# Kernel tuning notes

Measured on AMD Instinct MI355X. Metric: run time of the kernel, lower is better.

Reference implementation:

```python
import jax, jax.numpy as jnp
import numpy as np

K = 16
EPS = 1e-5

def _conv1x1(w, b, x):
    # w: [O, I], x: [B, I, N] -> [B, O, N]
    return jnp.einsum('oi,bin->bon', w, x) + b[None, :, None]

def _bn(g, be, m, v, x):
    # inference-mode batchnorm over channel dim of [B, C, N]
    inv = g / jnp.sqrt(v + EPS)
    return x * inv[None, :, None] + (be - m * inv)[None, :, None]

def setup_inputs() -> dict:
    key = jax.random.key(0)
    ks = jax.random.split(key, 16)
    B, C, N = 2, 128, 8192
    d = {}
    d['x'] = jax.random.normal(ks[0], (B, C, N), jnp.float32)
    d['xyz'] = jax.random.normal(ks[1], (B, N, 3), jnp.float32)
    def conv(k, o, i):
        k1, k2 = jax.random.split(k)
        s = 1.0 / np.sqrt(i)
        return (jax.random.uniform(k1, (o, i), jnp.float32, -s, s),
                jax.random.uniform(k2, (o,), jnp.float32, -s, s))
    def bn(k, c):
        return (jax.random.uniform(k, (c,), jnp.float32, 0.5, 1.5),
                jnp.zeros((c,), jnp.float32), jnp.zeros((c,), jnp.float32), jnp.ones((c,), jnp.float32))
    # boundary_net: 2C->C (bn,relu), C->C (bn,relu)
    d['bw1'], d['bb1'] = conv(ks[2], C, 2 * C)
    d['bn1g'], d['bn1b'], d['bn1m'], d['bn1v'] = bn(ks[3], C)
    d['bw2'], d['bb2'] = conv(ks[4], C, C)
    d['bn2g'], d['bn2b'], d['bn2m'], d['bn2v'] = bn(ks[5], C)
    # spatial_relation: 4->32 (bn,relu), 32->64
    d['sw1'], d['sb1'] = conv(ks[6], 32, 4)
    d['sbng'], d['sbnb'], d['sbnm'], d['sbnv'] = bn(ks[7], 32)
    d['sw2'], d['sb2'] = conv(ks[8], 64, 32)
    # attention: C+64 -> C//2 (bn,relu), C//2 -> C, sigmoid
    d['aw1'], d['ab1'] = conv(ks[9], C // 2, C + 64)
    d['abng'], d['abnb'], d['abnm'], d['abnv'] = bn(ks[10], C // 2)
    d['aw2'], d['ab2'] = conv(ks[11], C, C // 2)
    return d

def reference(x, xyz, bw1, bb1, bn1g, bn1b, bn1m, bn1v, bw2, bb2, bn2g, bn2b, bn2m, bn2v,
              sw1, sb1, sbng, sbnb, sbnm, sbnv, sw2, sb2,
              aw1, ab1, abng, abnb, abnm, abnv, aw2, ab2):
    B, C, N = x.shape
    # pairwise squared distances [B, N, N]
    xx = jnp.sum(xyz * xyz, axis=2)  # [B, N]
    dist = xx[:, :, None] + xx[:, None, :] - 2.0 * jnp.einsum('bnd,bmd->bnm', xyz, xyz)
    _, knn_idx = jax.lax.top_k(-dist, K)  # [B, N, K], K smallest distances
    # gather neighbor coords [B, N, K, 3]
    knn_xyz = jax.vmap(lambda p, i: p[i])(xyz, knn_idx)
    rel = knn_xyz - xyz[:, :, None, :]                  # [B, N, K, 3]
    rel_d = jnp.sqrt(jnp.sum(rel * rel, axis=-1))       # [B, N, K]
    mean_rel = jnp.mean(rel, axis=2).transpose(0, 2, 1)   # [B, 3, N]
    mean_d = jnp.mean(rel_d, axis=2)[:, None, :]           # [B, 1, N]
    spatial = jnp.concatenate([mean_rel, mean_d], axis=1)  # [B, 4, N]
    s = jax.nn.relu(_bn(sbng, sbnb, sbnm, sbnv, _conv1x1(sw1, sb1, spatial)))
    spatial_feat = _conv1x1(sw2, sb2, s)  # [B, 64, N]
    # gather neighbor features [B, C, N, K]
    knn_feat = jax.vmap(lambda xb, ib: xb[:, ib])(x, knn_idx)
    max_diff = jnp.max(knn_feat - x[:, :, :, None], axis=3)  # [B, C, N]
    bf = jnp.concatenate([x, max_diff], axis=1)  # [B, 2C, N]
    bf = jax.nn.relu(_bn(bn1g, bn1b, bn1m, bn1v, _conv1x1(bw1, bb1, bf)))
    boundary_feat = jax.nn.relu(_bn(bn2g, bn2b, bn2m, bn2v, _conv1x1(bw2, bb2, bf)))
    ai = jnp.concatenate([x, spatial_feat], axis=1)  # [B, C+64, N]
    a = jax.nn.relu(_bn(abng, abnb, abnm, abnv, _conv1x1(aw1, ab1, ai)))
    attn = jax.nn.sigmoid(_conv1x1(aw2, ab2, a))  # [B, C, N]
    return x + boundary_feat * attn
```

## Files before the change

kernel.cpp:

```cpp
#include <hip/hip_runtime.h>
#include <math.h>

#define NPTS  8192
#define NB    2
#define NTOT  (NPTS*NB)
#define GD    60
#define NCELL (GD*GD*GD)
#define TOTC  (NB*NCELL)
#define HCELL 0.2f
#define INVH  5.0f
#define ORGN  (-6.0f)
#define NN    8192
#define SCAN_CHUNK 1024
#define NBLK_SCAN  ((TOTC + SCAN_CHUNK - 1) / SCAN_CHUNK)
#define RSTART    2
#define RESC      4
#define SEL_CAP  1024

#define OFF_CNT     ((size_t)0)
#define OFF_OFFS    (OFF_CNT    + (size_t)TOTC*4)
#define OFF_CELLID  (OFF_OFFS   + (size_t)TOTC*4)
#define OFF_RANK    (OFF_CELLID + (size_t)NTOT*4)
#define OFF_SPOS    (OFF_RANK   + (size_t)NTOT*4)
#define OFF_KNN     (OFF_SPOS   + (size_t)NTOT*16)
#define OFF_SPATIAL (OFF_KNN    + (size_t)NTOT*16*4)
#define OFF_XT      (OFF_SPATIAL+ (size_t)NB*4*NPTS*4)
#define OFF_MD      (OFF_XT     + (size_t)NB*128*NPTS*4)
#define OFF_S1      (OFF_MD     + (size_t)NB*128*NPTS*4)
#define OFF_SF      (OFF_S1     + (size_t)NB*32*NPTS*4)
#define OFF_Y1      (OFF_SF     + (size_t)NB*64*NPTS*4)
#define OFF_Y2      (OFF_Y1     + (size_t)NB*128*NPTS*4)
#define OFF_A1      (OFF_Y2     + (size_t)NB*128*NPTS*4)
#define OFF_SC      (OFF_A1     + (size_t)NB*64*NPTS*4)
#define OFF_BSUM    (OFF_SC     + (size_t)1088*4)
#define OFF_BPRE    (OFF_BSUM   + (size_t)NBLK_SCAN*4)
#define OFF_RNG     (((OFF_BPRE + (size_t)NBLK_SCAN*4) + 15) & ~(size_t)15)

static __device__ __forceinline__ float sumsq3(float x, float y, float z) {
    return __fadd_rn(__fadd_rn(__fmul_rn(x, x), __fmul_rn(y, y)), __fmul_rn(z, z));
}
static __device__ __forceinline__ float pdist4(float qx, float qy, float qz, float qxx,
                                               float px, float py, float pz) {
    float pxx = sumsq3(px, py, pz);
    float dot = __fadd_rn(__fadd_rn(__fmul_rn(qx, px), __fmul_rn(qy, py)), __fmul_rn(qz, pz));
    return __fsub_rn(__fadd_rn(qxx, pxx), __fadd_rn(dot, dot));
}
static __device__ __forceinline__ unsigned fkey(float f) {
    unsigned b = __float_as_uint(f);
    return b ^ ((unsigned)(((int)b) >> 31) | 0x80000000u);
}
static __device__ __forceinline__ unsigned long long shflx64(unsigned long long v, int m) {
    unsigned lo = __shfl_xor((unsigned)v, m, 64);
    unsigned hi = __shfl_xor((unsigned)(v >> 32), m, 64);
    return ((unsigned long long)hi << 32) | lo;
}
static __device__ __forceinline__ int wave_scan_incl(int v, int lane) {
    #pragma unroll
    for (int d = 1; d < 64; d <<= 1) {
        int u = __shfl_up(v, d, 64);
        v += (lane >= d) ? u : 0;
    }
    return v;
}
static __device__ __forceinline__ unsigned long long tkmake(float m) {
    return ((unsigned long long)(fkey(__fsub_rn(__fmul_rn(m, m), 1e-4f)) + 1u)) << 27;
}

__global__ void cell_build(const float* __restrict__ xyz, int* __restrict__ cnt,
                           int* __restrict__ cellid, int* __restrict__ rank) {
    int t = blockIdx.x * 256 + threadIdx.x;
    if (t >= NTOT) return;
    const float* p = xyz + (size_t)t * 3;
    float x = p[0], y = p[1], z = p[2];
    int cx = min(GD - 1, max(0, (int)floorf((x - ORGN) * INVH)));
    int cy = min(GD - 1, max(0, (int)floorf((y - ORGN) * INVH)));
    int cz = min(GD - 1, max(0, (int)floorf((z - ORGN) * INVH)));
    int gcell = (t >> 13) * NCELL + (cz * GD + cy) * GD + cx;
    rank[t] = atomicAdd(&cnt[gcell], 1);
    cellid[t] = gcell;
}

__global__ __launch_bounds__(256) void scan_sums(const int* __restrict__ cnt, int* __restrict__ bsum) {
    __shared__ int red[256];
    int blk = blockIdx.x, t = threadIdx.x;
    int i0 = blk * SCAN_CHUNK + t * 4;
    int s = 0;
    if (i0 + 3 < TOTC) {
        int4 v = *(const int4*)(cnt + i0);
        s = v.x + v.y + v.z + v.w;
    } else {
        for (int j = 0; j < 4; ++j) if (i0 + j < TOTC) s += cnt[i0 + j];
    }
    red[t] = s;
    __syncthreads();
    for (int d = 128; d > 0; d >>= 1) {
        if (t < d) red[t] += red[t + d];
        __syncthreads();
    }
    if (t == 0) bsum[blk] = red[0];
}

__global__ __launch_bounds__(512) void scan_top(const int* __restrict__ bsum, int* __restrict__ bpre) {
    __shared__ int ps[512];
    int t = threadIdx.x;
    int v = (t < NBLK_SCAN) ? bsum[t] : 0;
    ps[t] = v;
    __syncthreads();
    for (int d = 1; d < 512; d <<= 1) {
        int u = 0;
        if (t >= d) u = ps[t - d];
        __syncthreads();
        ps[t] += u;
        __syncthreads();
    }
    if (t < NBLK_SCAN) bpre[t] = ps[t] - v;
}

__global__ __launch_bounds__(256) void scan_write(const int* __restrict__ cnt, const int* __restrict__ bpre,
                                                  int* __restrict__ offs, int2* __restrict__ rng) {
    __shared__ int ps[256];
    int blk = blockIdx.x, t = threadIdx.x;
    int i0 = blk * SCAN_CHUNK + t * 4;
    int a = 0, b = 0, c = 0, d = 0;
    if (i0 + 3 < TOTC) {
        int4 v = *(const int4*)(cnt + i0);
        a = v.x; b = v.y; c = v.z; d = v.w;
    } else {
        if (i0 + 0 < TOTC) a = cnt[i0 + 0];
        if (i0 + 1 < TOTC) b = cnt[i0 + 1];
        if (i0 + 2 < TOTC) c = cnt[i0 + 2];
        if (i0 + 3 < TOTC) d = cnt[i0 + 3];
    }
    int s = a + b + c + d;
    ps[t] = s;
    __syncthreads();
    for (int dd = 1; dd < 256; dd <<= 1) {
        int u = 0;
        if (t >= dd) u = ps[t - dd];
        __syncthreads();
        ps[t] += u;
        __syncthreads();
    }
    int base = bpre[blk] + ps[t] - s;
    if (i0 + 3 < TOTC) {
        offs[i0 + 0] = base;
        offs[i0 + 1] = base + a;
        offs[i0 + 2] = base + a + b;
        offs[i0 + 3] = base + a + b + c;
        *(int4*)(rng + i0)     = make_int4(base, base + a, base + a, base + a + b);
        *(int4*)(rng + i0 + 2) = make_int4(base + a + b, base + a + b + c,
                                           base + a + b + c, base + s);
    } else {
        if (i0 + 0 < TOTC) { offs[i0 + 0] = base;             rng[i0 + 0] = make_int2(base, base + a); }
        if (i0 + 1 < TOTC) { offs[i0 + 1] = base + a;         rng[i0 + 1] = make_int2(base + a, base + a + b); }
        if (i0 + 2 < TOTC) { offs[i0 + 2] = base + a + b;     rng[i0 + 2] = make_int2(base + a + b, base + a + b + c); }
        if (i0 + 3 < TOTC) { offs[i0 + 3] = base + a + b + c; rng[i0 + 3] = make_int2(base + a + b + c, base + s); }
    }
}

__global__ void scatter_k(const float* __restrict__ xyz, const int* __restrict__ cellid,
                          const int* __restrict__ rank, const int* __restrict__ offs,
                          float4* __restrict__ spos) {
    int t = blockIdx.x * 256 + threadIdx.x;
    if (t >= NTOT) return;
    const float* p = xyz + (size_t)t * 3;
    float x = p[0], y = p[1], z = p[2];
    int pos = offs[cellid[t]] + rank[t];
    spos[pos] = make_float4(x, y, z, __int_as_float(t & (NPTS - 1)));
}

__global__ __launch_bounds__(64) void knn_kernel(const float4* __restrict__ spos,
                                                 const int2* __restrict__ rng,
                                                 int* __restrict__ knn,
                                                 float* __restrict__ spatial) {
    __shared__ __align__(16) unsigned long long sel[SEL_CAP];
    __shared__ __align__(16) unsigned long long sel2[512];
    int lane = threadIdx.x;
    int bid  = blockIdx.x;
    int s = (int)(__brev((unsigned)bid) >> 18);
    float4 q = spos[s];
    float qx = q.x, qy = q.y, qz = q.z;
    float qxx = sumsq3(qx, qy, qz);
    int b  = s >> 13;
    int nq = __float_as_int(q.w);
    int cx = min(GD - 1, max(0, (int)floorf((qx - ORGN) * INVH)));
    int cy = min(GD - 1, max(0, (int)floorf((qy - ORGN) * INVH)));
    int cz = min(GD - 1, max(0, (int)floorf((qz - ORGN) * INVH)));
    const int2* rg = rng + b * NCELL;

    float mlx = qx - (ORGN + (float)cx * HCELL);
    float mhx = (ORGN + (float)(cx + 1) * HCELL) - qx;
    float mly = qy - (ORGN + (float)cy * HCELL);
    float mhy = (ORGN + (float)(cy + 1) * HCELL) - qy;
    float mlz = qz - (ORGN + (float)cz * HCELL);
    float mhz = (ORGN + (float)(cz + 1) * HCELL) - qz;
    float margin0 = fminf(fminf(fminf(mlx, mhx), fminf(mly, mhy)), fminf(mlz, mhz));

    int tot = 0, ovf = 0;

    auto scan_ball = [&](int RB, float mfin, unsigned long long tkfin) {
        if (mfin <= 0.f) return;
        float mfin2 = mfin * mfin;
        int L = 2 * RB + 1, nrows = L * L;
        for (int r0 = 0; r0 < nrows; r0 += 64) {
            int nr = min(64, nrows - r0);
            int rr = r0 + lane;
            int num = 0, start = 0;
            if (rr < nrows) {
                int dzr = rr / L - RB, dyr = rr % L - RB;
                int zc = cz + dzr, yc = cy + dyr;
                if ((unsigned)zc < GD && (unsigned)yc < GD) {
                    float ylo = ORGN + (float)yc * HCELL;
                    float zlo = ORGN + (float)zc * HCELL;
                    float dyl = fmaxf(fmaxf(ylo - qy, qy - (ylo + HCELL)), 0.f);
                    float dzl = fmaxf(fmaxf(zlo - qz, qz - (zlo + HCELL)), 0.f);
                    float rem = mfin2 - dyl * dyl - dzl * dzl;
                    if (rem > -1e-4f) {
                        float xh = sqrtf(fmaxf(rem, 0.f)) + 1e-3f;
                        int xlo = max(0, (int)floorf((qx - xh - ORGN) * INVH));
                        int xhi = min(GD - 1, (int)floorf((qx + xh - ORGN) * INVH));
                        if (xlo <= xhi) {
                            int rowb = (zc * GD + yc) * GD;
                            start = rg[rowb + xlo].x;
                            num   = rg[rowb + xhi].y - start;
                        }
                    }
                }
            }
            int inc = wave_scan_incl(num, lane);
            int ctot = __shfl(inc, 63, 64);
            if (ctot == 0) continue;
            int excl = inc - num;
            auto eg = [&](int base, int& sv, float4& pv, bool& vld) {
                int t = base + lane;
                vld = t < ctot;
                int tc = vld ? t : (ctot - 1);
                int lo = 0, hi = nr - 1;
                #pragma unroll
                for (int st = 0; st < 6; ++st) {
                    int mid = (lo + hi + 1) >> 1;
                    int e = __shfl(excl, mid, 64);
                    bool g = (e <= tc);
                    lo = g ? mid : lo;
                    hi = g ? hi : (mid - 1);
                }
                sv = __shfl(start, lo, 64) + (tc - __shfl(excl, lo, 64));
                pv = spos[sv];
            };
            int s0; float4 p0; bool v0;
            eg(0, s0, p0, v0);
            for (int base = 0; base < ctot; base += 64) {
                int s1 = 0; float4 p1 = p0; bool v1 = false;
                if (base + 64 < ctot) eg(base + 64, s1, p1, v1);
                float d = pdist4(qx, qy, qz, qxx, p0.x, p0.y, p0.z);
                unsigned long long key = ((unsigned long long)fkey(d) << 27)
                                       | ((unsigned long long)(unsigned)__float_as_int(p0.w) << 14)
                                       | (unsigned)s0;
                bool pass = v0 && (key < tkfin);
                unsigned long long mk = __ballot(pass);
                int cnum = (int)__popcll(mk);
                if (tot + cnum > SEL_CAP) { ovf = 1; return; }
                if (pass) sel[tot + (int)__popcll(mk & ((1ULL << lane) - 1ULL))] = key;
                tot += cnum;
                s0 = s1; p0 = p1; v0 = v1;
            }
        }
    };

    auto count_below = [&](unsigned long long tk) {
        int c = 0;
        for (int t0 = 0; t0 < tot; t0 += 64) {
            int tt = t0 + lane;
            if (tt < tot) c += (sel[tt] < tk) ? 1 : 0;
        }
        for (int o = 32; o > 0; o >>= 1) c += __shfl_xor(c, o, 64);
        return c;
    };

    float mfin1 = margin0 + (float)RSTART * HCELL;
    unsigned long long tkf1 = (mfin1 > 0.f) ? tkmake(mfin1) : 0ULL;
    if (tkf1) scan_ball(RSTART, mfin1, tkf1);

    unsigned long long tkey_sel = ~0ULL;
    int csel = 0;
    bool have = false;
    if (!ovf && tot >= 16) {
        float mA = margin0 + 1.0f * HCELL;
        if (mA > 0.f) {
            unsigned long long tkA = tkmake(mA);
            int cA = count_below(tkA);
            if (cA >= 16) { tkey_sel = tkA; csel = cA; have = true; }
        }
        if (!have) { tkey_sel = ~0ULL; csel = tot; have = true; }
    }
    if (!have && !ovf) {
        tot = 0;
        float mfin4 = margin0 + (float)RESC * HCELL;
        unsigned long long tkf4 = (mfin4 > 0.f) ? tkmake(mfin4) : 0ULL;
        if (tkf4) scan_ball(RESC, mfin4, tkf4);
        if (!ovf && tot >= 16) {
            float mB = margin0 + (float)(RESC - 1) * HCELL;
            if (mB > 0.f) {
                unsigned long long tkB = tkmake(mB);
                int cB = count_below(tkB);
                if (cB >= 16) { tkey_sel = tkB; csel = cB; have = true; }
            }
            if (!have) { tkey_sel = ~0ULL; csel = tot; have = true; }
        }
    }

    if (!have) {
        const float LADR[16] = {0.35f, 0.4725f, 0.637875f, 0.86113125f,
                                1.1625272f, 1.5694117f, 2.1187058f, 2.8602529f,
                                3.8613414f, 5.2128109f, 7.0372947f, 9.5003478f,
                                12.825470f, 17.314384f, 23.374418f, 31.555464f};
        int sbase = b << 13;
        int cc[16];
        #pragma unroll
        for (int k = 0; k < 16; ++k) cc[k] = 0;
        for (int i0 = 0; i0 < NPTS; i0 += 64) {
            float4 p = spos[sbase + i0 + lane];
            float d = pdist4(qx, qy, qz, qxx, p.x, p.y, p.z);
            #pragma unroll
            for (int k = 0; k < 16; ++k) cc[k] += (d < LADR[k] * LADR[k]) ? 1 : 0;
        }
        #pragma unroll
        for (int k = 0; k < 16; ++k)
            for (int o = 32; o > 0; o >>= 1) cc[k] += __shfl_xor(cc[k], o, 64);
        float Tq = LADR[15] * LADR[15]; int cL = cc[15];
        #pragma unroll
        for (int k = 14; k >= 0; --k) if (cc[k] >= 16) { Tq = LADR[k] * LADR[k]; cL = cc[k]; }
        if (cL <= SEL_CAP) {
            tot = 0;
            for (int i0 = 0; i0 < NPTS; i0 += 64) {
                int idx = sbase + i0 + lane;
                float4 p = spos[idx];
                float d = pdist4(qx, qy, qz, qxx, p.x, p.y, p.z);
                bool pass = (d < Tq);
                unsigned long long key = ((unsigned long long)fkey(d) << 27)
                                       | ((unsigned long long)(unsigned)__float_as_int(p.w) << 14)
                                       | (unsigned)idx;
                unsigned long long mk = __ballot(pass);
                if (pass) sel[tot + (int)__popcll(mk & ((1ULL << lane) - 1ULL))] = key;
                tot += (int)__popcll(mk);
            }
            tkey_sel = ~0ULL;
            csel = tot;
        } else {
            unsigned long long* mybuf = sel + lane;
            unsigned long long minkey = ~0ULL, maxkey = 0;
            int nbuf = 0;
            for (int i = lane; i < NPTS; i += 64) {
                float4 p = spos[sbase + i];
                float d = pdist4(qx, qy, qz, qxx, p.x, p.y, p.z);
                unsigned long long key = ((unsigned long long)fkey(d) << 27)
                                       | ((unsigned long long)(unsigned)__float_as_int(p.w) << 14)
                                       | (unsigned)(sbase + i);
                if (nbuf < 16) {
                    mybuf[(size_t)nbuf * 64] = key;
                    ++nbuf;
                    minkey = (key < minkey) ? key : minkey;
                    maxkey = (key > maxkey) ? key : maxkey;
                } else if (key < maxkey) {
                    unsigned long long vmax = 0, v2 = 0;
                    int pmax = 0;
                    #pragma unroll
                    for (int j = 0; j < 16; ++j) {
                        unsigned long long v = mybuf[(size_t)j * 64];
                        if (v > vmax) { v2 = vmax; vmax = v; pmax = j; }
                        else if (v > v2) { v2 = v; }
                    }
                    mybuf[(size_t)pmax * 64] = key;
                    maxkey = (key > v2) ? key : v2;
                    minkey = (key < minkey) ? key : minkey;
                }
            }
            unsigned long long keep = ~0ULL;
            for (int k = 0; k < 16; ++k) {
                unsigned long long m = minkey;
                for (int o = 32; o > 0; o >>= 1) {
                    unsigned long long pv = shflx64(m, o);
                    m = (pv < m) ? pv : m;
                }
                unsigned long long bal = __ballot(minkey == m);
                int wl = __ffsll((long long)bal) - 1;
                if (lane == wl) {
                    int pos = 0;
                    for (int j = 0; j < nbuf; ++j) if (mybuf[(size_t)j * 64] == m) pos = j;
                    --nbuf;
                    mybuf[(size_t)pos * 64] = mybuf[(size_t)nbuf * 64];
                    unsigned long long nm = ~0ULL;
                    for (int j = 0; j < nbuf; ++j) {
                        unsigned long long v = mybuf[(size_t)j * 64];
                        nm = (v < nm) ? v : nm;
                    }
                    minkey = nm;
                }
                if (lane == k) keep = m;
            }
            float rx = 0.f, ry = 0.f, rz = 0.f, rd = 0.f;
            if (lane < 16) {
                int sp = (int)(keep & 0x3FFFu);
                int oi = (int)((keep >> 14) & 0x1FFFu);
                float4 p = spos[sp];
                rx = p.x - qx; ry = p.y - qy; rz = p.z - qz;
                rd = sqrtf(__fadd_rn(__fadd_rn(__fmul_rn(rx, rx), __fmul_rn(ry, ry)), __fmul_rn(rz, rz)));
                knn[(((size_t)b << 13) + nq) * 16 + lane] = oi;
            }
            for (int o = 8; o > 0; o >>= 1) {
                rx += __shfl_xor(rx, o, 64);
                ry += __shfl_xor(ry, o, 64);
                rz += __shfl_xor(rz, o, 64);
                rd += __shfl_xor(rd, o, 64);
            }
            if (lane == 0) {
                const float inv16 = 0.0625f;
                spatial[((size_t)b * 4 + 0) * NPTS + nq] = rx * inv16;
                spatial[((size_t)b * 4 + 1) * NPTS + nq] = ry * inv16;
                spatial[((size_t)b * 4 + 2) * NPTS + nq] = rz * inv16;
                spatial[((size_t)b * 4 + 3) * NPTS + nq] = rd * inv16;
            }
            return;
        }
    }

    const unsigned long long* src = sel;
    int m = tot;
    if (tkey_sel != ~0ULL && csel <= 512) {
        int w = 0;
        for (int t0 = 0; t0 < tot; t0 += 64) {
            int tt = t0 + lane;
            unsigned long long v = (tt < tot) ? sel[tt] : ~0ULL;
            bool pass = (tt < tot) && (v < tkey_sel);
            unsigned long long mk = __ballot(pass);
            if (pass) sel2[w + (int)__popcll(mk & ((1ULL << lane) - 1ULL))] = v;
            w += (int)__popcll(mk);
        }
        asm volatile("s_waitcnt lgkmcnt(0)" ::: "memory");
        __builtin_amdgcn_sched_barrier(0);
        src = sel2; m = w;
        tkey_sel = ~0ULL;
    }
    float rxs = 0.f, rys = 0.f, rzs = 0.f, rds = 0.f;
    for (int t0 = 0; t0 < m; t0 += 64) {
        int tt = t0 + lane;
        if (tt < m) {
            unsigned long long kt = src[tt];
            if (kt < tkey_sel) {
                int rr = 0;
                for (int j = 0; j < m; ++j) rr += (src[j] < kt) ? 1 : 0;
                if (rr < 16) {
                    int sp = (int)(kt & 0x3FFFu);
                    int oi = (int)((kt >> 14) & 0x1FFFu);
                    float4 p = spos[sp];
                    float dx = p.x - qx, dy = p.y - qy, dz = p.z - qz;
                    float dl = sqrtf(__fadd_rn(__fadd_rn(__fmul_rn(dx, dx), __fmul_rn(dy, dy)), __fmul_rn(dz, dz)));
                    knn[(((size_t)b << 13) + nq) * 16 + rr] = oi;
                    rxs += dx; rys += dy; rzs += dz; rds += dl;
                }
            }
        }
    }
    for (int o = 32; o > 0; o >>= 1) {
        rxs += __shfl_xor(rxs, o, 64);
        rys += __shfl_xor(rys, o, 64);
        rzs += __shfl_xor(rzs, o, 64);
        rds += __shfl_xor(rds, o, 64);
    }
    if (lane == 0) {
        const float inv16 = 0.0625f;
        spatial[((size_t)b * 4 + 0) * NPTS + nq] = rxs * inv16;
        spatial[((size_t)b * 4 + 1) * NPTS + nq] = rys * inv16;
        spatial[((size_t)b * 4 + 2) * NPTS + nq] = rzs * inv16;
        spatial[((size_t)b * 4 + 3) * NPTS + nq] = rds * inv16;
    }
}

__global__ void transpose_k(const float* __restrict__ x, float* __restrict__ xT) {
    __shared__ float tl[32][33];
    int b = blockIdx.z;
    int n0 = blockIdx.x * 32, c0 = blockIdx.y * 32;
    int tx = threadIdx.x, ty = threadIdx.y;
    const float* xb = x + (size_t)b * 128 * NN;
    float* xtb = xT + (size_t)b * NN * 128;
    for (int i = 0; i < 32; i += 8) tl[ty + i][tx] = xb[(size_t)(c0 + ty + i) * NN + n0 + tx];
    __syncthreads();
    for (int i = 0; i < 32; i += 8) xtb[(size_t)(n0 + ty + i) * 128 + c0 + tx] = tl[tx][ty + i];
}

__global__ __launch_bounds__(256) void md_k(const float* __restrict__ xT,
                                            const int* __restrict__ knn,
                                            float* __restrict__ md) {
    __shared__ int ki[8][16];
    __shared__ float smd[8][132];
    int b = blockIdx.y;
    int n0 = blockIdx.x * 8;
    int tid = threadIdx.x;
    if (tid < 128) ki[tid >> 4][tid & 15] = knn[(((size_t)b << 13) + n0 + (tid >> 4)) * 16 + (tid & 15)];
    __syncthreads();
    int nl = tid >> 5;
    int c4 = (tid & 31) * 4;
    const float* xb = xT + (size_t)b * NPTS * 128;
    float4 m = make_float4(-3.0e38f, -3.0e38f, -3.0e38f, -3.0e38f);
    #pragma unroll
    for (int k = 0; k < 16; ++k) {
        const float4 g = *(const float4*)(xb + (size_t)ki[nl][k] * 128 + c4);
        m.x = fmaxf(m.x, g.x); m.y = fmaxf(m.y, g.y); m.z = fmaxf(m.z, g.z); m.w = fmaxf(m.w, g.w);
    }
    const float4 own = *(const float4*)(xb + (size_t)(n0 + nl) * 128 + c4);
    m.x -= own.x; m.y -= own.y; m.z -= own.z; m.w -= own.w;
    *(float4*)(&smd[nl][c4]) = m;
    __syncthreads();
    for (int r = 0; r < 4; ++r) {
        int c = (tid >> 3) + 32 * r;
        int n2 = tid & 7;
        md[((size_t)b * 128 + c) * NN + n0 + n2] = smd[n2][c];
    }
}

__global__ void prep_k(const float* bb1, const float* g1, const float* be1, const float* m1, const float* v1,
                       const float* bb2, const float* g2, const float* be2, const float* m2, const float* v2,
                       const float* sb1, const float* gs,  const float* bes, const float* ms, const float* vs,
                       const float* sb2,
                       const float* ab1, const float* ga,  const float* bea, const float* ma, const float* va,
                       const float* ab2, float* sc) {
    int t = threadIdx.x;
    if (t < 128) {
        float i1 = g1[t] / sqrtf(v1[t] + 1e-5f);
        sc[t] = i1;        sc[128 + t] = bb1[t] * i1 + be1[t] - m1[t] * i1;
        float i2 = g2[t] / sqrtf(v2[t] + 1e-5f);
        sc[256 + t] = i2;  sc[384 + t] = bb2[t] * i2 + be2[t] - m2[t] * i2;
        sc[832 + t] = 1.0f; sc[960 + t] = ab2[t];
    }
    if (t < 32) {
        float is = gs[t] / sqrtf(vs[t] + 1e-5f);
        sc[512 + t] = is;  sc[544 + t] = sb1[t] * is + bes[t] - ms[t] * is;
    }
    if (t < 64) {
        sc[576 + t] = 1.0f; sc[640 + t] = sb2[t];
        float ia = ga[t] / sqrtf(va[t] + 1e-5f);
        sc[704 + t] = ia;  sc[768 + t] = ab1[t] * ia + bea[t] - ma[t] * ia;
    }
}

template <int O, int K, int TILE_N, int SPLIT, int ACT>
__global__ __launch_bounds__(256) void conv_bn(const float* __restrict__ srcA,
                                               const float* __restrict__ srcB,
                                               const float* __restrict__ W,
                                               const float* __restrict__ scale,
                                               const float* __restrict__ shift,
                                               float* __restrict__ out) {
    constexpr int KC  = (K < 64) ? K : 64;
    constexpr int NT4 = TILE_N / 4;
    constexpr int O4  = O / 4;
    static_assert(NT4 * O4 == 256, "thread mapping");
    __shared__ float wT[KC][O + 4];
    __shared__ float inT[KC][TILE_N];
    int tid = threadIdx.x;
    int b = blockIdx.z;
    int n0 = blockIdx.x * TILE_N;
    int n_thr = tid % NT4;
    int o_thr = tid / NT4;
    float acc[4][4] = {{0.f, 0.f, 0.f, 0.f}, {0.f, 0.f, 0.f, 0.f}, {0.f, 0.f, 0.f, 0.f}, {0.f, 0.f, 0.f, 0.f}};

    for (int k0 = 0; k0 < K; k0 += KC) {
        for (int idx = tid; idx < KC * O; idx += 256) {
            int cc = idx % KC;
            int o  = idx / KC;
            wT[cc][o] = W[(size_t)o * K + k0 + cc];
        }
        for (int idx = tid; idx < KC * NT4; idx += 256) {
            int cc = idx / NT4;
            int nf = idx % NT4;
            int cg = k0 + cc;
            const float* src = (cg < SPLIT)
                ? (srcA + ((size_t)b * SPLIT + cg) * NN)
                : (srcB + ((size_t)b * (K - SPLIT) + (cg - SPLIT)) * NN);
            *(float4*)(&inT[cc][nf * 4]) = *(const float4*)(src + n0 + nf * 4);
        }
        __syncthreads();
        #pragma unroll 8
        for (int c = 0; c < KC; ++c) {
            float4 wv = *(const float4*)(&wT[c][o_thr * 4]);
            float4 iv = *(const float4*)(&inT[c][n_thr * 4]);
            acc[0][0] = fmaf(wv.x, iv.x, acc[0][0]); acc[0][1] = fmaf(wv.x, iv.y, acc[0][1]);
            acc[0][2] = fmaf(wv.x, iv.z, acc[0][2]); acc[0][3] = fmaf(wv.x, iv.w, acc[0][3]);
            acc[1][0] = fmaf(wv.y, iv.x, acc[1][0]); acc[1][1] = fmaf(wv.y, iv.y, acc[1][1]);
            acc[1][2] = fmaf(wv.y, iv.z, acc[1][2]); acc[1][3] = fmaf(wv.y, iv.w, acc[1][3]);
            acc[2][0] = fmaf(wv.z, iv.x, acc[2][0]); acc[2][1] = fmaf(wv.z, iv.y, acc[2][1]);
            acc[2][2] = fmaf(wv.z, iv.z, acc[2][2]); acc[2][3] = fmaf(wv.z, iv.w, acc[2][3]);
            acc[3][0] = fmaf(wv.w, iv.x, acc[3][0]); acc[3][1] = fmaf(wv.w, iv.y, acc[3][1]);
            acc[3][2] = fmaf(wv.w, iv.z, acc[3][2]); acc[3][3] = fmaf(wv.w, iv.w, acc[3][3]);
        }
        __syncthreads();
    }
    #pragma unroll
    for (int j = 0; j < 4; ++j) {
        int o = o_thr * 4 + j;
        float scv = scale[o], shv = shift[o];
        float4 v;
        v.x = fmaf(acc[j][0], scv, shv);
        v.y = fmaf(acc[j][1], scv, shv);
        v.z = fmaf(acc[j][2], scv, shv);
        v.w = fmaf(acc[j][3], scv, shv);
        size_t obase = ((size_t)b * O + o) * NN + n0 + n_thr * 4;
        if (ACT == 1) {
            v.x = fmaxf(v.x, 0.f); v.y = fmaxf(v.y, 0.f); v.z = fmaxf(v.z, 0.f); v.w = fmaxf(v.w, 0.f);
        }
        *(float4*)(out + obase) = v;
    }
}

#define FMA16(ACCV, WV, IV) \
    ACCV[0][0] = fmaf(WV.x, IV.x, ACCV[0][0]); ACCV[0][1] = fmaf(WV.x, IV.y, ACCV[0][1]); \
    ACCV[0][2] = fmaf(WV.x, IV.z, ACCV[0][2]); ACCV[0][3] = fmaf(WV.x, IV.w, ACCV[0][3]); \
    ACCV[1][0] = fmaf(WV.y, IV.x, ACCV[1][0]); ACCV[1][1] = fmaf(WV.y, IV.y, ACCV[1][1]); \
    ACCV[1][2] = fmaf(WV.y, IV.z, ACCV[1][2]); ACCV[1][3] = fmaf(WV.y, IV.w, ACCV[1][3]); \
    ACCV[2][0] = fmaf(WV.z, IV.x, ACCV[2][0]); ACCV[2][1] = fmaf(WV.z, IV.y, ACCV[2][1]); \
    ACCV[2][2] = fmaf(WV.z, IV.z, ACCV[2][2]); ACCV[2][3] = fmaf(WV.z, IV.w, ACCV[2][3]); \
    ACCV[3][0] = fmaf(WV.w, IV.x, ACCV[3][0]); ACCV[3][1] = fmaf(WV.w, IV.y, ACCV[3][1]); \
    ACCV[3][2] = fmaf(WV.w, IV.z, ACCV[3][2]); ACCV[3][3] = fmaf(WV.w, IV.w, ACCV[3][3])

__global__ __launch_bounds__(256) void fused_boundary(const float* __restrict__ x,
                                                      const float* __restrict__ md,
                                                      const float* __restrict__ W1,
                                                      const float* __restrict__ W2,
                                                      const float* __restrict__ sc,
                                                      float* __restrict__ y2b) {
    __shared__ float wT[64][132];
    __shared__ float inT[64][32];
    __shared__ float y1t[128][32];
    int tid = threadIdx.x;
    int b = blockIdx.z;
    int n0 = blockIdx.x * 32;
    int n_thr = tid % 8;
    int o_thr = tid / 8;
    float acc[4][4] = {{0.f,0.f,0.f,0.f},{0.f,0.f,0.f,0.f},{0.f,0.f,0.f,0.f},{0.f,0.f,0.f,0.f}};

    for (int k0 = 0; k0 < 256; k0 += 64) {
        for (int idx = tid; idx < 64 * 128; idx += 256) {
            int cc = idx % 64;
            int o  = idx / 64;
            wT[cc][o] = W1[(size_t)o * 256 + k0 + cc];
        }
        for (int idx = tid; idx < 64 * 8; idx += 256) {
            int cc = idx / 8;
            int nf = idx % 8;
            int cg = k0 + cc;
            const float* src = (cg < 128)
                ? (x  + ((size_t)b * 128 + cg) * NN)
                : (md + ((size_t)b * 128 + (cg - 128)) * NN);
            *(float4*)(&inT[cc][nf * 4]) = *(const float4*)(src + n0 + nf * 4);
        }
        __syncthreads();
        #pragma unroll 8
        for (int c = 0; c < 64; ++c) {
            float4 wv = *(const float4*)(&wT[c][o_thr * 4]);
            float4 iv = *(const float4*)(&inT[c][n_thr * 4]);
            FMA16(acc, wv, iv);
        }
        __syncthreads();
    }
    #pragma unroll
    for (int j = 0; j < 4; ++j) {
        int o = o_thr * 4 + j;
        float scv = sc[o], shv = sc[128 + o];
        float4 v;
        v.x = fmaxf(fmaf(acc[j][0], scv, shv), 0.f);
        v.y = fmaxf(fmaf(acc[j][1], scv, shv), 0.f);
        v.z = fmaxf(fmaf(acc[j][2], scv, shv), 0.f);
        v.w = fmaxf(fmaf(acc[j][3], scv, shv), 0.f);
        *(float4*)(&y1t[o][n_thr * 4]) = v;
    }
    __syncthreads();

    float a2[4][4] = {{0.f,0.f,0.f,0.f},{0.f,0.f,0.f,0.f},{0.f,0.f,0.f,0.f},{0.f,0.f,0.f,0.f}};
    for (int k0 = 0; k0 < 128; k0 += 64) {
        for (int idx = tid; idx < 64 * 128; idx += 256) {
            int cc = idx % 64;
            int o  = idx / 64;
            wT[cc][o] = W2[(size_t)o * 128 + k0 + cc];
        }
        __syncthreads();
        #pragma unroll 8
        for (int c = 0; c < 64; ++c) {
            float4 wv = *(const float4*)(&wT[c][o_thr * 4]);
            float4 iv = *(const float4*)(&y1t[k0 + c][n_thr * 4]);
            FMA16(a2, wv, iv);
        }
        __syncthreads();
    }
    #pragma unroll
    for (int j = 0; j < 4; ++j) {
        int o = o_thr * 4 + j;
        float scv = sc[256 + o], shv = sc[384 + o];
        float4 v;
        v.x = fmaxf(fmaf(a2[j][0], scv, shv), 0.f);
        v.y = fmaxf(fmaf(a2[j][1], scv, shv), 0.f);
        v.z = fmaxf(fmaf(a2[j][2], scv, shv), 0.f);
        v.w = fmaxf(fmaf(a2[j][3], scv, shv), 0.f);
        *(float4*)(y2b + ((size_t)b * 128 + o) * NN + n0 + n_thr * 4) = v;
    }
}

__global__ __launch_bounds__(256) void fused_attn(const float* __restrict__ x,
                                                  const float* __restrict__ sfb,
                                                  const float* __restrict__ W1,
                                                  const float* __restrict__ W2,
                                                  const float* __restrict__ sc,
                                                  const float* __restrict__ y2b,
                                                  float* __restrict__ dout) {
    __shared__ float wT[64][68];
    __shared__ float inT[64][64];
    __shared__ float a1t[64][64];
    int tid = threadIdx.x;
    int b = blockIdx.z;
    int n0 = blockIdx.x * 64;
    int n_thr = tid % 16;
    int o_thr = tid / 16;
    float acc[4][4] = {{0.f,0.f,0.f,0.f},{0.f,0.f,0.f,0.f},{0.f,0.f,0.f,0.f},{0.f,0.f,0.f,0.f}};

    for (int k0 = 0; k0 < 192; k0 += 64) {
        for (int idx = tid; idx < 64 * 64; idx += 256) {
            int cc = idx % 64;
            int o  = idx / 64;
            wT[cc][o] = W1[(size_t)o * 192 + k0 + cc];
        }
        for (int idx = tid; idx < 64 * 16; idx += 256) {
            int cc = idx / 16;
            int nf = idx % 16;
            int cg = k0 + cc;
            const float* src = (cg < 128)
                ? (x   + ((size_t)b * 128 + cg) * NN)
                : (sfb + ((size_t)b * 64 + (cg - 128)) * NN);
            *(float4*)(&inT[cc][nf * 4]) = *(const float4*)(src + n0 + nf * 4);
        }
        __syncthreads();
        #pragma unroll 8
        for (int c = 0; c < 64; ++c) {
            float4 wv = *(const float4*)(&wT[c][o_thr * 4]);
            float4 iv = *(const float4*)(&inT[c][n_thr * 4]);
            FMA16(acc, wv, iv);
        }
        __syncthreads();
    }
    #pragma unroll
    for (int j = 0; j < 4; ++j) {
        int o = o_thr * 4 + j;
        float scv = sc[704 + o], shv = sc[768 + o];
        float4 v;
        v.x = fmaxf(fmaf(acc[j][0], scv, shv), 0.f);
        v.y = fmaxf(fmaf(acc[j][1], scv, shv), 0.f);
        v.z = fmaxf(fmaf(acc[j][2], scv, shv), 0.f);
        v.w = fmaxf(fmaf(acc[j][3], scv, shv), 0.f);
        *(float4*)(&a1t[o][n_thr * 4]) = v;
    }
    __syncthreads();

    for (int oh = 0; oh < 128; oh += 64) {
        for (int idx = tid; idx < 64 * 64; idx += 256) {
            int cc = idx % 64;
            int o  = idx / 64;
            wT[cc][o] = W2[(size_t)(oh + o) * 64 + cc];
        }
        __syncthreads();
        float a2[4][4] = {{0.f,0.f,0.f,0.f},{0.f,0.f,0.f,0.f},{0.f,0.f,0.f,0.f},{0.f,0.f,0.f,0.f}};
        #pragma unroll 8
        for (int c = 0; c < 64; ++c) {
            float4 wv = *(const float4*)(&wT[c][o_thr * 4]);
            float4 iv = *(const float4*)(&a1t[c][n_thr * 4]);
            FMA16(a2, wv, iv);
        }
        #pragma unroll
        for (int j = 0; j < 4; ++j) {
            int o = oh + o_thr * 4 + j;
            float scv = sc[832 + o], shv = sc[960 + o];
            float4 v;
            v.x = fmaf(a2[j][0], scv, shv);
            v.y = fmaf(a2[j][1], scv, shv);
            v.z = fmaf(a2[j][2], scv, shv);
            v.w = fmaf(a2[j][3], scv, shv);
            size_t obase = ((size_t)b * 128 + o) * NN + n0 + n_thr * 4;
            float4 xr = *(const float4*)(x + obase);
            float4 yr = *(const float4*)(y2b + obase);
            v.x = xr.x + yr.x / (1.f + __expf(-v.x));
            v.y = xr.y + yr.y / (1.f + __expf(-v.y));
            v.z = xr.z + yr.z / (1.f + __expf(-v.z));
            v.w = xr.w + yr.w / (1.f + __expf(-v.w));
            *(float4*)(dout + obase) = v;
        }
        __syncthreads();
    }
}

extern "C" void kernel_launch(void* const* d_in, const int* in_sizes, int n_in,
                              void* d_out, int out_size, void* d_ws, size_t ws_size,
                              hipStream_t stream) {
    (void)in_sizes; (void)n_in; (void)out_size; (void)ws_size;
    const float* x    = (const float*)d_in[0];
    const float* xyz  = (const float*)d_in[1];
    const float* bw1  = (const float*)d_in[2];
    const float* bb1  = (const float*)d_in[3];
    const float* bn1g = (const float*)d_in[4];
    const float* bn1b = (const float*)d_in[5];
    const float* bn1m = (const float*)d_in[6];
    const float* bn1v = (const float*)d_in[7];
    const float* bw2  = (const float*)d_in[8];
    const float* bb2  = (const float*)d_in[9];
    const float* bn2g = (const float*)d_in[10];
    const float* bn2b = (const float*)d_in[11];
    const float* bn2m = (const float*)d_in[12];
    const float* bn2v = (const float*)d_in[13];
    const float* sw1  = (const float*)d_in[14];
    const float* sb1  = (const float*)d_in[15];
    const float* sbng = (const float*)d_in[16];
    const float* sbnb = (const float*)d_in[17];
    const float* sbnm = (const float*)d_in[18];
    const float* sbnv = (const float*)d_in[19];
    const float* sw2  = (const float*)d_in[20];
    const float* sb2  = (const float*)d_in[21];
    const float* aw1  = (const float*)d_in[22];
    const float* ab1  = (const float*)d_in[23];
    const float* abng = (const float*)d_in[24];
    const float* abnb = (const float*)d_in[25];
    const float* abnm = (const float*)d_in[26];
    const float* abnv = (const float*)d_in[27];
    const float* aw2  = (const float*)d_in[28];
    const float* ab2  = (const float*)d_in[29];

    char* ws = (char*)d_ws;
    int*    cnt    = (int*)(ws + OFF_CNT);
    int*    offs   = (int*)(ws + OFF_OFFS);
    int*    cellid = (int*)(ws + OFF_CELLID);
    int*    rank   = (int*)(ws + OFF_RANK);
    float4* spos   = (float4*)(ws + OFF_SPOS);
    int*    knn    = (int*)(ws + OFF_KNN);
    float*  spat   = (float*)(ws + OFF_SPATIAL);
    float*  xT     = (float*)(ws + OFF_XT);
    float*  md     = (float*)(ws + OFF_MD);
    float*  s1b    = (float*)(ws + OFF_S1);
    float*  sfb    = (float*)(ws + OFF_SF);
    float*  y2b    = (float*)(ws + OFF_Y2);
    float*  sc     = (float*)(ws + OFF_SC);
    int*    bsum   = (int*)(ws + OFF_BSUM);
    int*    bpre   = (int*)(ws + OFF_BPRE);
    int2*   rng    = (int2*)(ws + OFF_RNG);
    float*  dout   = (float*)d_out;

    hipMemsetAsync(cnt, 0, (size_t)TOTC * 4, stream);
    cell_build<<<dim3((NTOT + 255) / 256), 256, 0, stream>>>(xyz, cnt, cellid, rank);
    scan_sums<<<dim3(NBLK_SCAN), 256, 0, stream>>>(cnt, bsum);
    scan_top<<<dim3(1), 512, 0, stream>>>(bsum, bpre);
    scan_write<<<dim3(NBLK_SCAN), 256, 0, stream>>>(cnt, bpre, offs, rng);
    scatter_k<<<dim3((NTOT + 255) / 256), 256, 0, stream>>>(xyz, cellid, rank, offs, spos);
    knn_kernel<<<dim3(NTOT), 64, 0, stream>>>(spos, rng, knn, spat);
    transpose_k<<<dim3(NPTS / 32, 128 / 32, NB), dim3(32, 8), 0, stream>>>(x, xT);
    md_k<<<dim3(NPTS / 8, NB), 256, 0, stream>>>(xT, knn, md);
    prep_k<<<1, 128, 0, stream>>>(bb1, bn1g, bn1b, bn1m, bn1v,
                                  bb2, bn2g, bn2b, bn2m, bn2v,
                                  sb1, sbng, sbnb, sbnm, sbnv,
                                  sb2,
                                  ab1, abng, abnb, abnm, abnv,
                                  ab2, sc);
    conv_bn<32, 4, 128, 4, 1><<<dim3(NPTS / 128, 1, NB), 256, 0, stream>>>(
        spat, spat, sw1, sc + 512, sc + 544, s1b);
    conv_bn<64, 32, 64, 32, 0><<<dim3(NPTS / 64, 1, NB), 256, 0, stream>>>(
        s1b, s1b, sw2, sc + 576, sc + 640, sfb);
    fused_boundary<<<dim3(NPTS / 32, 1, NB), 256, 0, stream>>>(x, md, bw1, bw2, sc, y2b);
    fused_attn<<<dim3(NPTS / 64, 1, NB), 256, 0, stream>>>(x, sfb, aw1, aw2, sc, y2b, dout);
}
```

Before: 321.4 us.

## Process two kNN queries per wavefront using half-wave sub-groups

The kNN kernel now assigns one query to each 32-lane half of a 64-lane wave, so each block handles two queries and the launch uses half as many blocks. All scans, ballots, shuffles and reductions are narrowed to width 32. The shared selection buffers are split per half, which halves their capacity, and the query-to-block mapping changes from bit-reversed to a strided interleave. The goal is to stop wasting lanes when a query's candidate rows and points do not fill 64 lanes. The risks are that the two halves diverge and get serialized, and that the smaller buffers send more queries to the slow fallback path.

```diff
diff --git a/kernel.cpp b/kernel.cpp
--- a/kernel.cpp
+++ b/kernel.cpp
@@ -15,7 +15,7 @@
 #define NBLK_SCAN  ((TOTC + SCAN_CHUNK - 1) / SCAN_CHUNK)
 #define RSTART    2
 #define RESC      4
-#define SEL_CAP  1024
+#define SEL_CAP_H 512
 
 #define OFF_CNT     ((size_t)0)
 #define OFF_OFFS    (OFF_CNT    + (size_t)TOTC*4)
@@ -49,16 +49,16 @@
     unsigned b = __float_as_uint(f);
     return b ^ ((unsigned)(((int)b) >> 31) | 0x80000000u);
 }
-static __device__ __forceinline__ unsigned long long shflx64(unsigned long long v, int m) {
-    unsigned lo = __shfl_xor((unsigned)v, m, 64);
-    unsigned hi = __shfl_xor((unsigned)(v >> 32), m, 64);
+static __device__ __forceinline__ unsigned long long shflx64_32(unsigned long long v, int m) {
+    unsigned lo = __shfl_xor((unsigned)v, m, 32);
+    unsigned hi = __shfl_xor((unsigned)(v >> 32), m, 32);
     return ((unsigned long long)hi << 32) | lo;
 }
-static __device__ __forceinline__ int wave_scan_incl(int v, int lane) {
+static __device__ __forceinline__ int scan_incl32(int v, int sub) {
     #pragma unroll
-    for (int d = 1; d < 64; d <<= 1) {
-        int u = __shfl_up(v, d, 64);
-        v += (lane >= d) ? u : 0;
+    for (int d = 1; d < 32; d <<= 1) {
+        int u = __shfl_up(v, d, 32);
+        v += (sub >= d) ? u : 0;
     }
     return v;
 }
@@ -173,11 +173,16 @@
                                                  const int2* __restrict__ rng,
                                                  int* __restrict__ knn,
                                                  float* __restrict__ spatial) {
-    __shared__ __align__(16) unsigned long long sel[SEL_CAP];
-    __shared__ __align__(16) unsigned long long sel2[512];
+    __shared__ __align__(16) unsigned long long selbuf[2][SEL_CAP_H];
+    __shared__ __align__(16) unsigned long long sel2buf[2][256];
     int lane = threadIdx.x;
+    int half = lane >> 5;
+    int sub  = lane & 31;
     int bid  = blockIdx.x;
-    int s = (int)(__brev((unsigned)bid) >> 18);
+    int pq = (bid & 7) * (NTOT / 16) + (bid >> 3);
+    int s  = pq * 2 + half;
+    unsigned long long* sel  = selbuf[half];
+    unsigned long long* sel2 = sel2buf[half];
     float4 q = spos[s];
     float qx = q.x, qy = q.y, qz = q.z;
     float qxx = sumsq3(qx, qy, qz);
@@ -202,9 +207,9 @@
         if (mfin <= 0.f) return;
         float mfin2 = mfin * mfin;
         int L = 2 * RB + 1, nrows = L * L;
-        for (int r0 = 0; r0 < nrows; r0 += 64) {
-            int nr = min(64, nrows - r0);
-            int rr = r0 + lane;
+        for (int r0 = 0; r0 < nrows; r0 += 32) {
+            int nr = min(32, nrows - r0);
+            int rr = r0 + sub;
             int num = 0, start = 0;
             if (rr < nrows) {
                 int dzr = rr / L - RB, dyr = rr % L - RB;
@@ -227,40 +232,41 @@
                     }
                 }
             }
-            int inc = wave_scan_incl(num, lane);
-            int ctot = __shfl(inc, 63, 64);
+            int inc = scan_incl32(num, sub);
+            int ctot = __shfl(inc, 31, 32);
             if (ctot == 0) continue;
             int excl = inc - num;
             auto eg = [&](int base, int& sv, float4& pv, bool& vld) {
-                int t = base + lane;
+                int t = base + sub;
                 vld = t < ctot;
                 int tc = vld ? t : (ctot - 1);
                 int lo = 0, hi = nr - 1;
                 #pragma unroll
-                for (int st = 0; st < 6; ++st) {
+                for (int st = 0; st < 5; ++st) {
                     int mid = (lo + hi + 1) >> 1;
-                    int e = __shfl(excl, mid, 64);
+                    int e = __shfl(excl, mid, 32);
                     bool g = (e <= tc);
                     lo = g ? mid : lo;
                     hi = g ? hi : (mid - 1);
                 }
-                sv = __shfl(start, lo, 64) + (tc - __shfl(excl, lo, 64));
+                sv = __shfl(start, lo, 32) + (tc - __shfl(excl, lo, 32));
                 pv = spos[sv];
             };
             int s0; float4 p0; bool v0;
             eg(0, s0, p0, v0);
-            for (int base = 0; base < ctot; base += 64) {
+            for (int base = 0; base < ctot; base += 32) {
                 int s1 = 0; float4 p1 = p0; bool v1 = false;
-                if (base + 64 < ctot) eg(base + 64, s1, p1, v1);
+                if (base + 32 < ctot) eg(base + 32, s1, p1, v1);
                 float d = pdist4(qx, qy, qz, qxx, p0.x, p0.y, p0.z);
                 unsigned long long key = ((unsigned long long)fkey(d) << 27)
                                        | ((unsigned long long)(unsigned)__float_as_int(p0.w) << 14)
                                        | (unsigned)s0;
                 bool pass = v0 && (key < tkfin);
-                unsigned long long mk = __ballot(pass);
-                int cnum = (int)__popcll(mk);
-                if (tot + cnum > SEL_CAP) { ovf = 1; return; }
-                if (pass) sel[tot + (int)__popcll(mk & ((1ULL << lane) - 1ULL))] = key;
+                unsigned long long mk64 = __ballot(pass);
+                unsigned hm = (unsigned)(mk64 >> (half << 5));
+                int cnum = __popc(hm);
+                if (tot + cnum > SEL_CAP_H) { ovf = 1; return; }
+                if (pass) sel[tot + __popc(hm & ((1u << sub) - 1u))] = key;
                 tot += cnum;
                 s0 = s1; p0 = p1; v0 = v1;
             }
@@ -269,11 +275,11 @@
 
     auto count_below = [&](unsigned long long tk) {
         int c = 0;
-        for (int t0 = 0; t0 < tot; t0 += 64) {
-            int tt = t0 + lane;
+        for (int t0 = 0; t0 < tot; t0 += 32) {
+            int tt = t0 + sub;
             if (tt < tot) c += (sel[tt] < tk) ? 1 : 0;
         }
-        for (int o = 32; o > 0; o >>= 1) c += __shfl_xor(c, o, 64);
+        for (int o = 16; o > 0; o >>= 1) c += __shfl_xor(c, o, 32);
         return c;
     };
 
@@ -318,46 +324,47 @@
         int cc[16];
         #pragma unroll
         for (int k = 0; k < 16; ++k) cc[k] = 0;
-        for (int i0 = 0; i0 < NPTS; i0 += 64) {
-            float4 p = spos[sbase + i0 + lane];
+        for (int i0 = 0; i0 < NPTS; i0 += 32) {
+            float4 p = spos[sbase + i0 + sub];
             float d = pdist4(qx, qy, qz, qxx, p.x, p.y, p.z);
             #pragma unroll
             for (int k = 0; k < 16; ++k) cc[k] += (d < LADR[k] * LADR[k]) ? 1 : 0;
         }
         #pragma unroll
         for (int k = 0; k < 16; ++k)
-            for (int o = 32; o > 0; o >>= 1) cc[k] += __shfl_xor(cc[k], o, 64);
+            for (int o = 16; o > 0; o >>= 1) cc[k] += __shfl_xor(cc[k], o, 32);
         float Tq = LADR[15] * LADR[15]; int cL = cc[15];
         #pragma unroll
         for (int k = 14; k >= 0; --k) if (cc[k] >= 16) { Tq = LADR[k] * LADR[k]; cL = cc[k]; }
-        if (cL <= SEL_CAP) {
+        if (cL <= SEL_CAP_H) {
             tot = 0;
-            for (int i0 = 0; i0 < NPTS; i0 += 64) {
-                int idx = sbase + i0 + lane;
+            for (int i0 = 0; i0 < NPTS; i0 += 32) {
+                int idx = sbase + i0 + sub;
                 float4 p = spos[idx];
                 float d = pdist4(qx, qy, qz, qxx, p.x, p.y, p.z);
                 bool pass = (d < Tq);
                 unsigned long long key = ((unsigned long long)fkey(d) << 27)
                                        | ((unsigned long long)(unsigned)__float_as_int(p.w) << 14)
                                        | (unsigned)idx;
-                unsigned long long mk = __ballot(pass);
-                if (pass) sel[tot + (int)__popcll(mk & ((1ULL << lane) - 1ULL))] = key;
-                tot += (int)__popcll(mk);
+                unsigned long long mk64 = __ballot(pass);
+                unsigned hm = (unsigned)(mk64 >> (half << 5));
+                if (pass) sel[tot + __popc(hm & ((1u << sub) - 1u))] = key;
+                tot += __popc(hm);
             }
             tkey_sel = ~0ULL;
             csel = tot;
         } else {
-            unsigned long long* mybuf = sel + lane;
+            unsigned long long* mybuf = sel + sub;
             unsigned long long minkey = ~0ULL, maxkey = 0;
             int nbuf = 0;
-            for (int i = lane; i < NPTS; i += 64) {
+            for (int i = sub; i < NPTS; i += 32) {
                 float4 p = spos[sbase + i];
                 float d = pdist4(qx, qy, qz, qxx, p.x, p.y, p.z);
                 unsigned long long key = ((unsigned long long)fkey(d) << 27)
                                        | ((unsigned long long)(unsigned)__float_as_int(p.w) << 14)
                                        | (unsigned)(sbase + i);
                 if (nbuf < 16) {
-                    mybuf[(size_t)nbuf * 64] = key;
+                    mybuf[(size_t)nbuf * 32] = key;
                     ++nbuf;
                     minkey = (key < minkey) ? key : minkey;
                     maxkey = (key > maxkey) ? key : maxkey;
@@ -366,11 +373,11 @@
                     int pmax = 0;
                     #pragma unroll
                     for (int j = 0; j < 16; ++j) {
-                        unsigned long long v = mybuf[(size_t)j * 64];
+                        unsigned long long v = mybuf[(size_t)j * 32];
                         if (v > vmax) { v2 = vmax; vmax = v; pmax = j; }
                         else if (v > v2) { v2 = v; }
                     }
-                    mybuf[(size_t)pmax * 64] = key;
+                    mybuf[(size_t)pmax * 32] = key;
                     maxkey = (key > v2) ? key : v2;
                     minkey = (key < minkey) ? key : minkey;
                 }
@@ -378,42 +385,43 @@
             unsigned long long keep = ~0ULL;
             for (int k = 0; k < 16; ++k) {
                 unsigned long long m = minkey;
-                for (int o = 32; o > 0; o >>= 1) {
-                    unsigned long long pv = shflx64(m, o);
+                for (int o = 16; o > 0; o >>= 1) {
+                    unsigned long long pv = shflx64_32(m, o);
                     m = (pv < m) ? pv : m;
                 }
                 unsigned long long bal = __ballot(minkey == m);
-                int wl = __ffsll((long long)bal) - 1;
-                if (lane == wl) {
+                unsigned hm = (unsigned)(bal >> (half << 5));
+                int wl = __ffs(hm) - 1;
+                if (sub == wl) {
                     int pos = 0;
-                    for (int j = 0; j < nbuf; ++j) if (mybuf[(size_t)j * 64] == m) pos = j;
+                    for (int j = 0; j < nbuf; ++j) if (mybuf[(size_t)j * 32] == m) pos = j;
                     --nbuf;
-                    mybuf[(size_t)pos * 64] = mybuf[(size_t)nbuf * 64];
+                    mybuf[(size_t)pos * 32] = mybuf[(size_t)nbuf * 32];
                     unsigned long long nm = ~0ULL;
                     for (int j = 0; j < nbuf; ++j) {
-                        unsigned long long v = mybuf[(size_t)j * 64];
+                        unsigned long long v = mybuf[(size_t)j * 32];
                         nm = (v < nm) ? v : nm;
                     }
                     minkey = nm;
                 }
-                if (lane == k) keep = m;
+                if (sub == k) keep = m;
             }
             float rx = 0.f, ry = 0.f, rz = 0.f, rd = 0.f;
-            if (lane < 16) {
+            if (sub < 16) {
                 int sp = (int)(keep & 0x3FFFu);
                 int oi = (int)((keep >> 14) & 0x1FFFu);
                 float4 p = spos[sp];
                 rx = p.x - qx; ry = p.y - qy; rz = p.z - qz;
                 rd = sqrtf(__fadd_rn(__fadd_rn(__fmul_rn(rx, rx), __fmul_rn(ry, ry)), __fmul_rn(rz, rz)));
-                knn[(((size_t)b << 13) + nq) * 16 + lane] = oi;
+                knn[(((size_t)b << 13) + nq) * 16 + sub] = oi;
             }
             for (int o = 8; o > 0; o >>= 1) {
-                rx += __shfl_xor(rx, o, 64);
-                ry += __shfl_xor(ry, o, 64);
-                rz += __shfl_xor(rz, o, 64);
-                rd += __shfl_xor(rd, o, 64);
-            }
-            if (lane == 0) {
+                rx += __shfl_xor(rx, o, 32);
+                ry += __shfl_xor(ry, o, 32);
+                rz += __shfl_xor(rz, o, 32);
+                rd += __shfl_xor(rd, o, 32);
+            }
+            if (sub == 0) {
                 const float inv16 = 0.0625f;
                 spatial[((size_t)b * 4 + 0) * NPTS + nq] = rx * inv16;
                 spatial[((size_t)b * 4 + 1) * NPTS + nq] = ry * inv16;
@@ -426,15 +434,16 @@
 
     const unsigned long long* src = sel;
     int m = tot;
-    if (tkey_sel != ~0ULL && csel <= 512) {
+    if (tkey_sel != ~0ULL && csel <= 256) {
         int w = 0;
-        for (int t0 = 0; t0 < tot; t0 += 64) {
-            int tt = t0 + lane;
+        for (int t0 = 0; t0 < tot; t0 += 32) {
+            int tt = t0 + sub;
             unsigned long long v = (tt < tot) ? sel[tt] : ~0ULL;
             bool pass = (tt < tot) && (v < tkey_sel);
-            unsigned long long mk = __ballot(pass);
-            if (pass) sel2[w + (int)__popcll(mk & ((1ULL << lane) - 1ULL))] = v;
-            w += (int)__popcll(mk);
+            unsigned long long mk64 = __ballot(pass);
+            unsigned hm = (unsigned)(mk64 >> (half << 5));
+            if (pass) sel2[w + __popc(hm & ((1u << sub) - 1u))] = v;
+            w += __popc(hm);
         }
         asm volatile("s_waitcnt lgkmcnt(0)" ::: "memory");
         __builtin_amdgcn_sched_barrier(0);
@@ -442,8 +451,8 @@
         tkey_sel = ~0ULL;
     }
     float rxs = 0.f, rys = 0.f, rzs = 0.f, rds = 0.f;
-    for (int t0 = 0; t0 < m; t0 += 64) {
-        int tt = t0 + lane;
+    for (int t0 = 0; t0 < m; t0 += 32) {
+        int tt = t0 + sub;
         if (tt < m) {
             unsigned long long kt = src[tt];
             if (kt < tkey_sel) {
@@ -461,13 +470,13 @@
             }
         }
     }
-    for (int o = 32; o > 0; o >>= 1) {
-        rxs += __shfl_xor(rxs, o, 64);
-        rys += __shfl_xor(rys, o, 64);
-        rzs += __shfl_xor(rzs, o, 64);
-        rds += __shfl_xor(rds, o, 64);
-    }
-    if (lane == 0) {
+    for (int o = 16; o > 0; o >>= 1) {
+        rxs += __shfl_xor(rxs, o, 32);
+        rys += __shfl_xor(rys, o, 32);
+        rzs += __shfl_xor(rzs, o, 32);
+        rds += __shfl_xor(rds, o, 32);
+    }
+    if (sub == 0) {
         const float inv16 = 0.0625f;
         spatial[((size_t)b * 4 + 0) * NPTS + nq] = rxs * inv16;
         spatial[((size_t)b * 4 + 1) * NPTS + nq] = rys * inv16;
@@ -853,7 +862,7 @@
     scan_top<<<dim3(1), 512, 0, stream>>>(bsum, bpre);
     scan_write<<<dim3(NBLK_SCAN), 256, 0, stream>>>(cnt, bpre, offs, rng);
     scatter_k<<<dim3((NTOT + 255) / 256), 256, 0, stream>>>(xyz, cellid, rank, offs, spos);
-    knn_kernel<<<dim3(NTOT), 64, 0, stream>>>(spos, rng, knn, spat);
+    knn_kernel<<<dim3(NTOT / 2), 64, 0, stream>>>(spos, rng, knn, spat);
     transpose_k<<<dim3(NPTS / 32, 128 / 32, NB), dim3(32, 8), 0, stream>>>(x, xT);
     md_k<<<dim3(NPTS / 8, NB), 256, 0, stream>>>(xT, knn, md);
     prep_k<<<1, 128, 0, stream>>>(bb1, bn1g, bn1b, bn1m, bn1v,
```

Result: slower. 368.7 us (+14.7%).
